# Kernel tuning notes

Hardware: AMD Instinct MI355X
Metric: run time of the kernel (lower is better)

## Reference

```python
import jax, jax.numpy as jnp
import numpy as np

B, S, T = 64, 512, 32
H2 = 1024          # hidden_size * 2
ATT = 512          # attention_size


def setup_inputs() -> dict:
    key = jax.random.key(0)
    k1, k2, k3, k4, k5, k6 = jax.random.split(key, 6)
    h = jax.random.normal(k1, (B, S, H2), dtype=jnp.float32)
    h_mask = jax.random.randint(k2, (B, S), 0, 2).astype(jnp.int32)
    ht = jax.random.normal(k3, (B, T, H2), dtype=jnp.float32)
    # Linear params (xavier-ish scale)
    w1_w = jax.random.normal(k4, (ATT, 2 * H2), dtype=jnp.float32) * (1.0 / np.sqrt(2 * H2))
    w1_b = jax.random.normal(k5, (ATT,), dtype=jnp.float32) * 0.02
    u_w = jax.random.normal(k6, (1, ATT), dtype=jnp.float32) * (1.0 / np.sqrt(ATT))
    return {"h": h, "h_mask": h_mask, "ht": ht, "w1_w": w1_w, "w1_b": w1_b, "u_w": u_w}


def reference(h, h_mask, ht, w1_w, w1_b, u_w):
    # h: [B,S,2H], ht: [B,T,2H], h_mask: [B,S] (1 = valid, 0 = pad)
    valid = h_mask != 0                                  # [B,S]
    ht_mean = jnp.mean(ht, axis=1, keepdims=True)        # [B,1,2H]
    h_cat = jnp.concatenate(
        [h, jnp.broadcast_to(ht_mean, h.shape)], axis=2)  # [B,S,4H]
    h_cat = jnp.where(valid[..., None], h_cat, 0.0)
    a = jnp.tanh(jnp.einsum('bsf,af->bsa', h_cat, w1_w) + w1_b)  # [B,S,ATT]
    a = jnp.where(valid[..., None], a, 0.0)
    beta = jnp.einsum('bsa,a->bs', a, u_w[0])            # [B,S]
    beta = jnp.where(valid, beta, -1e20)
    alpha = jax.nn.softmax(beta, axis=1)                 # [B,S]
    s = jnp.einsum('bs,bsd->bd', alpha, h)               # [B,2H]
    return s
```

## Files before the change

### kernel.cpp

```cpp
#include <hip/hip_runtime.h>
#include <math.h>
#include <stdint.h>

#define Bb 64
#define Ss 512
#define Tt 32
#define H2 1024
#define FF 2048
#define ATT 512
#define MM (Bb * Ss)

typedef short bf8 __attribute__((ext_vector_type(8)));
typedef float f4 __attribute__((ext_vector_type(4)));

__device__ __forceinline__ unsigned short f2bf(float f) {
    unsigned u = __float_as_uint(f);
    u = (u + 0x7fffu + ((u >> 16) & 1u)) >> 16;
    return (unsigned short)u;
}

__device__ __forceinline__ void gl_lds16(const void* g, void* l) {
    __builtin_amdgcn_global_load_lds((const __attribute__((address_space(1))) void*)g,
                                     (__attribute__((address_space(3))) void*)l, 16, 0, 0);
}

__device__ __forceinline__ float tanh_fast(float x) {
    return 1.0f - 2.0f / (__expf(2.0f * x) + 1.0f);
}

__global__ void init_kernel(float* __restrict__ beta, float* __restrict__ out) {
    int i = blockIdx.x * 256 + threadIdx.x;
    if (i < Bb * Ss) beta[i] = 0.0f;
    if (i < Bb * H2) out[i] = 0.0f;
}

__global__ void mean_kernel(const float* __restrict__ ht, float* __restrict__ ht_mean) {
    int b = blockIdx.x;
    int d4 = threadIdx.x;
    const float4* p = (const float4*)(ht + (size_t)b * Tt * H2);
    float4 acc = make_float4(0.f, 0.f, 0.f, 0.f);
    #pragma unroll 4
    for (int t = 0; t < Tt; ++t) {
        float4 v = p[(size_t)t * (H2 / 4) + d4];
        acc.x += v.x; acc.y += v.y; acc.z += v.z; acc.w += v.w;
    }
    const float inv = 1.0f / (float)Tt;
    acc.x *= inv; acc.y *= inv; acc.z *= inv; acc.w *= inv;
    ((float4*)(ht_mean + (size_t)b * H2))[d4] = acc;
}

__global__ __launch_bounds__(256) void c2_kernel2(const float* __restrict__ ht_mean,
                                                  const float* __restrict__ w1_w,
                                                  const float* __restrict__ w1_b,
                                                  float* __restrict__ c2) {
    __shared__ float hm[H2];
    int b = blockIdx.x;
    for (int i = threadIdx.x; i < H2; i += 256) hm[i] = ht_mean[(size_t)b * H2 + i];
    __syncthreads();
    int a = blockIdx.y * 64 + ((int)threadIdx.x >> 2);
    int q = (int)threadIdx.x & 3;
    const float4* w   = (const float4*)(w1_w + (size_t)a * FF + H2 + q * 256);
    const float4* hm4 = (const float4*)(hm + q * 256);
    float acc = 0.f;
    #pragma unroll 8
    for (int k = 0; k < 64; ++k) {
        float4 wv = w[k]; float4 hv = hm4[k];
        acc += wv.x * hv.x + wv.y * hv.y + wv.z * hv.z + wv.w * hv.w;
    }
    acc += __shfl_xor(acc, 1);
    acc += __shfl_xor(acc, 2);
    if (q == 0) c2[(size_t)b * ATT + a] = acc + w1_b[a];
}

__global__ void convw_kernel(const float* __restrict__ w1_w, unsigned short* __restrict__ out) {
    size_t e = ((size_t)blockIdx.x * 256 + threadIdx.x) * 8;
    int row = (int)(e >> 10);
    int c = (int)(e & 1023);
    const float* src = w1_w + (size_t)row * FF + c;
    float4 a = *(const float4*)(src);
    float4 b = *(const float4*)(src + 4);
    bf8 v = { (short)f2bf(a.x), (short)f2bf(a.y), (short)f2bf(a.z), (short)f2bf(a.w),
              (short)f2bf(b.x), (short)f2bf(b.y), (short)f2bf(b.z), (short)f2bf(b.w) };
    *(bf8*)(out + e) = v;
}

__global__ void convh_kernel(const float* __restrict__ in, unsigned short* __restrict__ out) {
    size_t i = ((size_t)blockIdx.x * 256 + threadIdx.x) * 8;
    float4 a = *(const float4*)(in + i);
    float4 b = *(const float4*)(in + i + 4);
    bf8 v = { (short)f2bf(a.x), (short)f2bf(a.y), (short)f2bf(a.z), (short)f2bf(a.w),
              (short)f2bf(b.x), (short)f2bf(b.y), (short)f2bf(b.z), (short)f2bf(b.w) };
    *(bf8*)(out + i) = v;
}

__global__ __launch_bounds__(256, 4) void gemm_m97_kernel(
        const unsigned short* __restrict__ hb, const unsigned short* __restrict__ wb,
        const float* __restrict__ c2, const float* __restrict__ u_w,
        float* __restrict__ beta) {
    __shared__ __align__(16) unsigned short As[2][128 * 32];
    __shared__ __align__(16) unsigned short Bs[2][128 * 32];

    const int id = (int)blockIdx.x;
    const int wg = (id & 7) * 128 + (id >> 3);
    const int mt = wg >> 2, nt = wg & 3;
    const int m0 = mt * 128, n0 = nt * 128;

    const int tid = (int)threadIdx.x;
    const int wid = tid >> 6, lane = tid & 63;
    const int wr = (wid >> 1) * 64, wc = (wid & 1) * 64;
    const int col = lane & 15, rg = lane >> 4;
    const int rswz = rg ^ ((col >> 1) & 3);

    f4 acc[4][4] = {};

    const int srow = tid >> 2;
    const int sslot = (tid & 3) ^ ((tid >> 3) & 3);
    const unsigned short* Agl = hb + (size_t)(m0 + srow) * H2 + sslot * 8;
    const unsigned short* Bgl = wb + (size_t)(n0 + srow) * H2 + sslot * 8;
    const int ldsb = wid * 512;

    gl_lds16(Agl,                   &As[0][ldsb]);
    gl_lds16(Agl + (size_t)64 * H2, &As[0][ldsb + 2048]);
    gl_lds16(Bgl,                   &Bs[0][ldsb]);
    gl_lds16(Bgl + (size_t)64 * H2, &Bs[0][ldsb + 2048]);
    __syncthreads();

    int cur = 0;
    for (int t = 0; t < 32; ++t) {
        if (t < 31) {
            const int kn = (t + 1) * 32;
            gl_lds16(Agl + kn,                   &As[cur ^ 1][ldsb]);
            gl_lds16(Agl + kn + (size_t)64 * H2, &As[cur ^ 1][ldsb + 2048]);
            gl_lds16(Bgl + kn,                   &Bs[cur ^ 1][ldsb]);
            gl_lds16(Bgl + kn + (size_t)64 * H2, &Bs[cur ^ 1][ldsb + 2048]);
        }
        __builtin_amdgcn_sched_barrier(0);
        bf8 av[4], bv[4];
        #pragma unroll
        for (int i = 0; i < 4; ++i) {
            av[i] = *(const bf8*)&As[cur][(wr + i * 16 + col) * 32 + rswz * 8];
            bv[i] = *(const bf8*)&Bs[cur][(wc + i * 16 + col) * 32 + rswz * 8];
        }
        #pragma unroll
        for (int i = 0; i < 4; ++i)
            #pragma unroll
            for (int j = 0; j < 4; ++j)
                acc[i][j] = __builtin_amdgcn_mfma_f32_16x16x32_bf16(av[i], bv[j], acc[i][j], 0, 0, 0);
        __syncthreads();
        cur ^= 1;
    }

    const int b_idx = mt >> 2;
    const float* c2b = c2 + (size_t)b_idx * ATT + n0 + wc;
    const float* ub  = u_w + n0 + wc;
    float rp[4][4] = {};
    #pragma unroll
    for (int j = 0; j < 4; ++j) {
        int n = j * 16 + col;
        float cv = c2b[n];
        float uv = ub[n];
        #pragma unroll
        for (int i = 0; i < 4; ++i)
            #pragma unroll
            for (int r = 0; r < 4; ++r)
                rp[i][r] += tanh_fast(acc[i][j][r] + cv) * uv;
    }
    #pragma unroll
    for (int i = 0; i < 4; ++i)
        #pragma unroll
        for (int r = 0; r < 4; ++r) {
            float v = rp[i][r];
            v += __shfl_xor(v, 1);
            v += __shfl_xor(v, 2);
            v += __shfl_xor(v, 4);
            v += __shfl_xor(v, 8);
            if (col == 0)
                atomicAdd(&beta[(size_t)m0 + wr + i * 16 + rg * 4 + r], v);
        }
}

__global__ void softmax_kernel(const float* __restrict__ beta, const int* __restrict__ h_mask,
                               float* __restrict__ alpha) {
    __shared__ float red[16];
    int b = blockIdx.x;
    int s = (int)threadIdx.x;
    float v = (h_mask[(size_t)b * Ss + s] != 0) ? beta[(size_t)b * Ss + s] : -1e20f;
    float m = v;
    #pragma unroll
    for (int off = 32; off >= 1; off >>= 1) m = fmaxf(m, __shfl_xor(m, off, 64));
    int wave = s >> 6;
    if ((s & 63) == 0) red[wave] = m;
    __syncthreads();
    float mx = red[0];
    #pragma unroll
    for (int w = 1; w < 8; ++w) mx = fmaxf(mx, red[w]);
    float e = expf(v - mx);
    float sum = e;
    #pragma unroll
    for (int off = 32; off >= 1; off >>= 1) sum += __shfl_xor(sum, off, 64);
    __syncthreads();
    if ((s & 63) == 0) red[8 + wave] = sum;
    __syncthreads();
    float tot = 0.f;
    #pragma unroll
    for (int w = 0; w < 8; ++w) tot += red[8 + w];
    alpha[(size_t)b * Ss + s] = e / tot;
}

__global__ void wsum_bf_kernel(const unsigned short* __restrict__ hb,
                               const float* __restrict__ alpha, float* __restrict__ out) {
    int b = blockIdx.x;
    int g = (int)threadIdx.x >> 7;
    int t = (int)threadIdx.x & 127;
    int d0 = t * 8;
    int s0 = blockIdx.y * 64 + g * 32;
    const unsigned short* hp = hb + (size_t)b * Ss * H2 + (size_t)s0 * H2 + d0;
    const float* ap = alpha + (size_t)b * Ss + s0;
    float acc[8] = {};
    #pragma unroll 4
    for (int s = 0; s < 32; ++s) {
        bf8 v = *(const bf8*)(hp + (size_t)s * H2);
        float a = ap[s];
        #pragma unroll
        for (int j = 0; j < 8; ++j) {
            float hv = __uint_as_float(((unsigned)(unsigned short)v[j]) << 16);
            acc[j] = fmaf(a, hv, acc[j]);
        }
    }
    #pragma unroll
    for (int j = 0; j < 8; ++j)
        atomicAdd(&out[(size_t)b * H2 + d0 + j], acc[j]);
}

extern "C" void kernel_launch(void* const* d_in, const int* in_sizes, int n_in,
                              void* d_out, int out_size, void* d_ws, size_t ws_size,
                              hipStream_t stream) {
    const float* h      = (const float*)d_in[0];
    const int*   h_mask = (const int*)d_in[1];
    const float* ht     = (const float*)d_in[2];
    const float* w1_w   = (const float*)d_in[3];
    const float* w1_b   = (const float*)d_in[4];
    const float* u_w    = (const float*)d_in[5];
    float* out = (float*)d_out;

    float* ws      = (float*)d_ws;
    float* ht_mean = ws;
    float* c2      = ws + 65536;
    float* beta    = ws + 98304;
    float* alpha   = ws + 131072;
    unsigned short* w1a_bf = (unsigned short*)((char*)d_ws + 659456);
    unsigned short* h_bf   = (unsigned short*)((char*)d_ws + 659456 + 1048576);

    hipLaunchKernelGGL(init_kernel, dim3(256), dim3(256), 0, stream, beta, out);
    hipLaunchKernelGGL(mean_kernel, dim3(Bb), dim3(256), 0, stream, ht, ht_mean);
    hipLaunchKernelGGL(c2_kernel2, dim3(Bb, 8), dim3(256), 0, stream, ht_mean, w1_w, w1_b, c2);
    hipLaunchKernelGGL(convw_kernel, dim3(256), dim3(256), 0, stream, w1_w, w1a_bf);
    hipLaunchKernelGGL(convh_kernel, dim3(16384), dim3(256), 0, stream, h, h_bf);
    hipLaunchKernelGGL(gemm_m97_kernel, dim3((MM / 128) * (ATT / 128)), dim3(256), 0, stream,
                       h_bf, w1a_bf, c2, u_w, beta);
    hipLaunchKernelGGL(softmax_kernel, dim3(Bb), dim3(512), 0, stream, beta, h_mask, alpha);
    hipLaunchKernelGGL(wsum_bf_kernel, dim3(Bb, 8), dim3(256), 0, stream, h_bf, alpha, out);
}
```

Measured before the change: 336.5 us.

## Merge prep kernels, triple-buffer GEMM loads, fuse softmax into weighted sum

Init, mean and weight-conversion kernels are merged into one prep launch. The GEMM moves from double to triple buffering, with two tiles in flight and explicit vmcnt waits instead of a full syncthreads. Softmax is folded into the weighted-sum kernel, where each block recomputes the row softmax and keeps its slice of alpha in LDS. This removes launches and the alpha round trip, at the cost of redundant softmax work and more LDS per block, which lowers GEMM occupancy.

```diff
diff --git a/kernel.cpp b/kernel.cpp
--- a/kernel.cpp
+++ b/kernel.cpp
@@ -28,25 +28,38 @@
     return 1.0f - 2.0f / (__expf(2.0f * x) + 1.0f);
 }
 
-__global__ void init_kernel(float* __restrict__ beta, float* __restrict__ out) {
-    int i = blockIdx.x * 256 + threadIdx.x;
-    if (i < Bb * Ss) beta[i] = 0.0f;
-    if (i < Bb * H2) out[i] = 0.0f;
-}
-
-__global__ void mean_kernel(const float* __restrict__ ht, float* __restrict__ ht_mean) {
-    int b = blockIdx.x;
-    int d4 = threadIdx.x;
-    const float4* p = (const float4*)(ht + (size_t)b * Tt * H2);
-    float4 acc = make_float4(0.f, 0.f, 0.f, 0.f);
-    #pragma unroll 4
-    for (int t = 0; t < Tt; ++t) {
-        float4 v = p[(size_t)t * (H2 / 4) + d4];
-        acc.x += v.x; acc.y += v.y; acc.z += v.z; acc.w += v.w;
-    }
-    const float inv = 1.0f / (float)Tt;
-    acc.x *= inv; acc.y *= inv; acc.z *= inv; acc.w *= inv;
-    ((float4*)(ht_mean + (size_t)b * H2))[d4] = acc;
+__global__ __launch_bounds__(256) void prep_kernel(
+        const float* __restrict__ ht, float* __restrict__ ht_mean,
+        const float* __restrict__ w1_w, unsigned short* __restrict__ w1a_bf,
+        float* __restrict__ beta, float* __restrict__ out) {
+    const int bx = (int)blockIdx.x, tid = (int)threadIdx.x;
+    if (bx < 384) {
+        int i = bx * 256 + tid;
+        if (i < Bb * Ss) beta[i] = 0.0f;
+        else out[i - Bb * Ss] = 0.0f;
+    } else if (bx < 448) {
+        int b = bx - 384;
+        const float4* p = (const float4*)(ht + (size_t)b * Tt * H2);
+        float4 acc = make_float4(0.f, 0.f, 0.f, 0.f);
+        #pragma unroll 4
+        for (int t = 0; t < Tt; ++t) {
+            float4 v = p[(size_t)t * (H2 / 4) + tid];
+            acc.x += v.x; acc.y += v.y; acc.z += v.z; acc.w += v.w;
+        }
+        const float inv = 1.0f / (float)Tt;
+        acc.x *= inv; acc.y *= inv; acc.z *= inv; acc.w *= inv;
+        ((float4*)(ht_mean + (size_t)b * H2))[tid] = acc;
+    } else {
+        size_t e = ((size_t)(bx - 448) * 256 + tid) * 8;
+        int row = (int)(e >> 10);
+        int c = (int)(e & 1023);
+        const float* src = w1_w + (size_t)row * FF + c;
+        float4 a = *(const float4*)(src);
+        float4 b = *(const float4*)(src + 4);
+        bf8 v = { (short)f2bf(a.x), (short)f2bf(a.y), (short)f2bf(a.z), (short)f2bf(a.w),
+                  (short)f2bf(b.x), (short)f2bf(b.y), (short)f2bf(b.z), (short)f2bf(b.w) };
+        *(bf8*)(w1a_bf + e) = v;
+    }
 }
 
 __global__ __launch_bounds__(256) void c2_kernel2(const float* __restrict__ ht_mean,
@@ -72,18 +85,6 @@
     if (q == 0) c2[(size_t)b * ATT + a] = acc + w1_b[a];
 }
 
-__global__ void convw_kernel(const float* __restrict__ w1_w, unsigned short* __restrict__ out) {
-    size_t e = ((size_t)blockIdx.x * 256 + threadIdx.x) * 8;
-    int row = (int)(e >> 10);
-    int c = (int)(e & 1023);
-    const float* src = w1_w + (size_t)row * FF + c;
-    float4 a = *(const float4*)(src);
-    float4 b = *(const float4*)(src + 4);
-    bf8 v = { (short)f2bf(a.x), (short)f2bf(a.y), (short)f2bf(a.z), (short)f2bf(a.w),
-              (short)f2bf(b.x), (short)f2bf(b.y), (short)f2bf(b.z), (short)f2bf(b.w) };
-    *(bf8*)(out + e) = v;
-}
-
 __global__ void convh_kernel(const float* __restrict__ in, unsigned short* __restrict__ out) {
     size_t i = ((size_t)blockIdx.x * 256 + threadIdx.x) * 8;
     float4 a = *(const float4*)(in + i);
@@ -93,12 +94,12 @@
     *(bf8*)(out + i) = v;
 }
 
-__global__ __launch_bounds__(256, 4) void gemm_m97_kernel(
+__global__ __launch_bounds__(256, 3) void gemm_p3_kernel(
         const unsigned short* __restrict__ hb, const unsigned short* __restrict__ wb,
         const float* __restrict__ c2, const float* __restrict__ u_w,
         float* __restrict__ beta) {
-    __shared__ __align__(16) unsigned short As[2][128 * 32];
-    __shared__ __align__(16) unsigned short Bs[2][128 * 32];
+    __shared__ __align__(16) unsigned short As[3][128 * 32];
+    __shared__ __align__(16) unsigned short Bs[3][128 * 32];
 
     const int id = (int)blockIdx.x;
     const int wg = (id & 7) * 128 + (id >> 3);
@@ -119,20 +120,26 @@
     const unsigned short* Bgl = wb + (size_t)(n0 + srow) * H2 + sslot * 8;
     const int ldsb = wid * 512;
 
-    gl_lds16(Agl,                   &As[0][ldsb]);
-    gl_lds16(Agl + (size_t)64 * H2, &As[0][ldsb + 2048]);
-    gl_lds16(Bgl,                   &Bs[0][ldsb]);
-    gl_lds16(Bgl + (size_t)64 * H2, &Bs[0][ldsb + 2048]);
-    __syncthreads();
+    #pragma unroll
+    for (int p = 0; p < 2; ++p) {
+        const int k0 = p * 32;
+        gl_lds16(Agl + k0,                   &As[p][ldsb]);
+        gl_lds16(Agl + k0 + (size_t)64 * H2, &As[p][ldsb + 2048]);
+        gl_lds16(Bgl + k0,                   &Bs[p][ldsb]);
+        gl_lds16(Bgl + k0 + (size_t)64 * H2, &Bs[p][ldsb + 2048]);
+    }
+    asm volatile("s_waitcnt vmcnt(4)" ::: "memory");
+    __builtin_amdgcn_s_barrier();
 
     int cur = 0;
     for (int t = 0; t < 32; ++t) {
-        if (t < 31) {
-            const int kn = (t + 1) * 32;
-            gl_lds16(Agl + kn,                   &As[cur ^ 1][ldsb]);
-            gl_lds16(Agl + kn + (size_t)64 * H2, &As[cur ^ 1][ldsb + 2048]);
-            gl_lds16(Bgl + kn,                   &Bs[cur ^ 1][ldsb]);
-            gl_lds16(Bgl + kn + (size_t)64 * H2, &Bs[cur ^ 1][ldsb + 2048]);
+        if (t < 30) {
+            int wrb = cur + 2; if (wrb >= 3) wrb -= 3;
+            const int kn = (t + 2) * 32;
+            gl_lds16(Agl + kn,                   &As[wrb][ldsb]);
+            gl_lds16(Agl + kn + (size_t)64 * H2, &As[wrb][ldsb + 2048]);
+            gl_lds16(Bgl + kn,                   &Bs[wrb][ldsb]);
+            gl_lds16(Bgl + kn + (size_t)64 * H2, &Bs[wrb][ldsb + 2048]);
         }
         __builtin_amdgcn_sched_barrier(0);
         bf8 av[4], bv[4];
@@ -146,8 +153,10 @@
             #pragma unroll
             for (int j = 0; j < 4; ++j)
                 acc[i][j] = __builtin_amdgcn_mfma_f32_16x16x32_bf16(av[i], bv[j], acc[i][j], 0, 0, 0);
-        __syncthreads();
-        cur ^= 1;
+        if (t < 30) asm volatile("s_waitcnt vmcnt(4)" ::: "memory");
+        else        asm volatile("s_waitcnt vmcnt(0)" ::: "memory");
+        __builtin_amdgcn_s_barrier();
+        cur = (cur == 2) ? 0 : cur + 1;
     }
 
     const int b_idx = mt >> 2;
@@ -179,48 +188,46 @@
         }
 }
 
-__global__ void softmax_kernel(const float* __restrict__ beta, const int* __restrict__ h_mask,
-                               float* __restrict__ alpha) {
-    __shared__ float red[16];
-    int b = blockIdx.x;
-    int s = (int)threadIdx.x;
-    float v = (h_mask[(size_t)b * Ss + s] != 0) ? beta[(size_t)b * Ss + s] : -1e20f;
-    float m = v;
-    #pragma unroll
-    for (int off = 32; off >= 1; off >>= 1) m = fmaxf(m, __shfl_xor(m, off, 64));
-    int wave = s >> 6;
-    if ((s & 63) == 0) red[wave] = m;
-    __syncthreads();
-    float mx = red[0];
-    #pragma unroll
-    for (int w = 1; w < 8; ++w) mx = fmaxf(mx, red[w]);
-    float e = expf(v - mx);
-    float sum = e;
-    #pragma unroll
-    for (int off = 32; off >= 1; off >>= 1) sum += __shfl_xor(sum, off, 64);
-    __syncthreads();
-    if ((s & 63) == 0) red[8 + wave] = sum;
-    __syncthreads();
-    float tot = 0.f;
-    #pragma unroll
-    for (int w = 0; w < 8; ++w) tot += red[8 + w];
-    alpha[(size_t)b * Ss + s] = e / tot;
-}
-
-__global__ void wsum_bf_kernel(const unsigned short* __restrict__ hb,
-                               const float* __restrict__ alpha, float* __restrict__ out) {
-    int b = blockIdx.x;
-    int g = (int)threadIdx.x >> 7;
-    int t = (int)threadIdx.x & 127;
-    int d0 = t * 8;
-    int s0 = blockIdx.y * 64 + g * 32;
-    const unsigned short* hp = hb + (size_t)b * Ss * H2 + (size_t)s0 * H2 + d0;
-    const float* ap = alpha + (size_t)b * Ss + s0;
+__global__ __launch_bounds__(256) void wsum2_kernel(
+        const unsigned short* __restrict__ hb, const float* __restrict__ beta,
+        const int* __restrict__ h_mask, float* __restrict__ out) {
+    __shared__ float red[8];
+    __shared__ float al[64];
+    const int b = (int)blockIdx.x;
+    const int sc = (int)blockIdx.y;
+    const int tid = (int)threadIdx.x;
+    const int lane = tid & 63, wave = tid >> 6;
+
+    const float* bp = beta + (size_t)b * Ss;
+    const int* mp = h_mask + (size_t)b * Ss;
+    float v1 = mp[tid]       ? bp[tid]       : -1e20f;
+    float v2 = mp[tid + 256] ? bp[tid + 256] : -1e20f;
+    float mx = fmaxf(v1, v2);
+    #pragma unroll
+    for (int off = 32; off >= 1; off >>= 1) mx = fmaxf(mx, __shfl_xor(mx, off, 64));
+    if (lane == 0) red[wave] = mx;
+    __syncthreads();
+    mx = fmaxf(fmaxf(red[0], red[1]), fmaxf(red[2], red[3]));
+    float e1 = __expf(v1 - mx), e2 = __expf(v2 - mx);
+    float sm = e1 + e2;
+    #pragma unroll
+    for (int off = 32; off >= 1; off >>= 1) sm += __shfl_xor(sm, off, 64);
+    if (lane == 0) red[4 + wave] = sm;
+    __syncthreads();
+    const float inv = 1.0f / ((red[4] + red[5]) + (red[6] + red[7]));
+    int ls1 = tid - sc * 64, ls2 = tid + 256 - sc * 64;
+    if ((unsigned)ls1 < 64u) al[ls1] = e1 * inv;
+    if ((unsigned)ls2 < 64u) al[ls2] = e2 * inv;
+    __syncthreads();
+
+    const int g = tid >> 7, t = tid & 127;
+    const int d0 = t * 8, si = g * 32;
+    const unsigned short* hp = hb + ((size_t)b * Ss + sc * 64 + si) * H2 + d0;
     float acc[8] = {};
     #pragma unroll 4
     for (int s = 0; s < 32; ++s) {
         bf8 v = *(const bf8*)(hp + (size_t)s * H2);
-        float a = ap[s];
+        float a = al[si + s];
         #pragma unroll
         for (int j = 0; j < 8; ++j) {
             float hv = __uint_as_float(((unsigned)(unsigned short)v[j]) << 16);
@@ -247,17 +254,14 @@
     float* ht_mean = ws;
     float* c2      = ws + 65536;
     float* beta    = ws + 98304;
-    float* alpha   = ws + 131072;
     unsigned short* w1a_bf = (unsigned short*)((char*)d_ws + 659456);
     unsigned short* h_bf   = (unsigned short*)((char*)d_ws + 659456 + 1048576);
 
-    hipLaunchKernelGGL(init_kernel, dim3(256), dim3(256), 0, stream, beta, out);
-    hipLaunchKernelGGL(mean_kernel, dim3(Bb), dim3(256), 0, stream, ht, ht_mean);
+    hipLaunchKernelGGL(prep_kernel, dim3(704), dim3(256), 0, stream,
+                       ht, ht_mean, w1_w, w1a_bf, beta, out);
     hipLaunchKernelGGL(c2_kernel2, dim3(Bb, 8), dim3(256), 0, stream, ht_mean, w1_w, w1_b, c2);
-    hipLaunchKernelGGL(convw_kernel, dim3(256), dim3(256), 0, stream, w1_w, w1a_bf);
     hipLaunchKernelGGL(convh_kernel, dim3(16384), dim3(256), 0, stream, h, h_bf);
-    hipLaunchKernelGGL(gemm_m97_kernel, dim3((MM / 128) * (ATT / 128)), dim3(256), 0, stream,
+    hipLaunchKernelGGL(gemm_p3_kernel, dim3((MM / 128) * (ATT / 128)), dim3(256), 0, stream,
                        h_bf, w1a_bf, c2, u_w, beta);
-    hipLaunchKernelGGL(softmax_kernel, dim3(Bb), dim3(512), 0, stream, beta, h_mask, alpha);
-    hipLaunchKernelGGL(wsum_bf_kernel, dim3(Bb, 8), dim3(256), 0, stream, h_bf, alpha, out);
-}
+    hipLaunchKernelGGL(wsum2_kernel, dim3(Bb, 8), dim3(256), 0, stream, h_bf, beta, h_mask, out);
+}
```

Result: no change. 342.8 us (+1.9%).
